# Performance work log

Hardware: AMD Instinct MI355X
Metric: run time of the kernel (lower is better)

The kernel has to match this reference:

```python
import jax, jax.numpy as jnp
import numpy as np

N, D_IN, D_OUT = 16384, 1024, 1024
E, R, TOP_K = 8, 16, 2
ALPHA = 32.0
SCALING = ALPHA / R  # standard LoRA scaling alpha/rank


def setup_inputs() -> dict:
    key = jax.random.key(0)
    k_tok, k_wb, k_a, k_b, k_g = jax.random.split(key, 5)
    tokens = jax.random.normal(k_tok, (N, D_IN), dtype=jnp.float32)
    # frozen attention projection
    W_base = jax.random.normal(k_wb, (D_IN, D_OUT), dtype=jnp.float32) * (1.0 / np.sqrt(D_IN))
    # per-expert LoRA factors
    A = jax.random.normal(k_a, (E, D_IN, R), dtype=jnp.float32) * 0.02
    B = jax.random.normal(k_b, (E, R, D_OUT), dtype=jnp.float32) * 0.02
    # router
    W_gate = jax.random.normal(k_g, (D_IN, E), dtype=jnp.float32) * (1.0 / np.sqrt(D_IN))
    return {"tokens": tokens, "W_base": W_base, "A": A, "B": B, "W_gate": W_gate}


def reference(tokens, W_base, A, B, W_gate):
    # Router: top-k gating with softmax over the selected logits
    router_logits = tokens @ W_gate                      # [N, E]
    topk_vals, selected_experts = jax.lax.top_k(router_logits, TOP_K)  # [N, K]
    expert_weights = jax.nn.softmax(topk_vals, axis=-1)  # [N, K]

    # Dense combine weights: zeros except selected experts
    gates = jnp.zeros((tokens.shape[0], E), dtype=tokens.dtype)
    gates = gates.at[jnp.arange(tokens.shape[0])[:, None], selected_experts].set(expert_weights)  # [N, E]

    # Frozen base projection
    base_out = tokens @ W_base                           # [N, D_out]

    # LoRA experts: low-rank intermediate [N, E, R] is small (rank 16)
    h = jnp.einsum('nd,edr->ner', tokens, A)             # [N, E, R]
    h = h * gates[:, :, None]                            # gate before expanding to D_out
    lora_out = jnp.einsum('ner,erm->nm', h, B)           # [N, D_out]

    out = base_out + SCALING * lora_out
    return out, router_logits, selected_experts, expert_weights
```

## Files before the change

kernel.cpp:

```cpp
#include <hip/hip_runtime.h>
#include <hip/hip_bf16.h>
#include <cstdint>
#include <cfloat>

#define NTOK 16384
#define DIN  1024
#define DOUT 1024
#define NEXP 8
#define RLORA 16
#define KTOT 1152
#define SCALE_LORA 2.0f

typedef __attribute__((ext_vector_type(8))) short bf16x8;
typedef __attribute__((ext_vector_type(4))) float f32x4;

__device__ __forceinline__ unsigned short f2bf(float f) {
  __hip_bfloat16 h = __float2bfloat16(f);
  unsigned short u;
  __builtin_memcpy(&u, &h, 2);
  return u;
}

__device__ __forceinline__ void gld_lds16(const void* g, void* l) {
  __builtin_amdgcn_global_load_lds((const __attribute__((address_space(1))) void*)g,
                                   (__attribute__((address_space(3))) void*)l,
                                   16, 0, 0);
}

__global__ __launch_bounds__(256) void k_transW(const float* __restrict__ Wb,
                                                const float* __restrict__ B,
                                                unsigned short* __restrict__ WcatT) {
  __shared__ unsigned short T[64][66];
  const int k0 = blockIdx.x * 64, j0 = blockIdx.y * 64;
  const int t = threadIdx.x;
#pragma unroll
  for (int p = 0; p < 4; ++p) {
    int kk = p * 16 + (t >> 4);
    int c4 = (t & 15) * 4;
    int k = k0 + kk;
    const float* src = (k < 1024) ? (Wb + (size_t)k * 1024) : (B + (size_t)(k - 1024) * 1024);
    float4 v = *(const float4*)(src + j0 + c4);
    T[kk][c4 + 0] = f2bf(v.x); T[kk][c4 + 1] = f2bf(v.y);
    T[kk][c4 + 2] = f2bf(v.z); T[kk][c4 + 3] = f2bf(v.w);
  }
  __syncthreads();
#pragma unroll
  for (int p = 0; p < 2; ++p) {
    int jj = p * 32 + (t >> 3);
    int kc = (t & 7) * 8;
    unsigned short buf[8];
#pragma unroll
    for (int i = 0; i < 8; ++i) buf[i] = T[kc + i][jj];
    uint4 u; __builtin_memcpy(&u, buf, 16);
    *(uint4*)(WcatT + (size_t)(j0 + jj) * KTOT + k0 + kc) = u;
  }
}

__global__ __launch_bounds__(256) void k_transA(const float* __restrict__ A,
                                                unsigned short* __restrict__ AcatT) {
  __shared__ unsigned short T[256][17];
  const int e = blockIdx.y, d0 = blockIdx.x * 256;
  const int t = threadIdx.x;
#pragma unroll
  for (int p = 0; p < 4; ++p) {
    int idx = p * 256 + t;
    int d = idx >> 2;
    int rr = (idx & 3) * 4;
    float4 v = *(const float4*)(A + (size_t)e * 16384 + (size_t)(d0 + d) * 16 + rr);
    T[d][rr + 0] = f2bf(v.x); T[d][rr + 1] = f2bf(v.y);
    T[d][rr + 2] = f2bf(v.z); T[d][rr + 3] = f2bf(v.w);
  }
  __syncthreads();
#pragma unroll
  for (int p = 0; p < 2; ++p) {
    int slot = p * 256 + t;
    int r = slot >> 5;
    int dc = (slot & 31) * 8;
    unsigned short buf[8];
#pragma unroll
    for (int i = 0; i < 8; ++i) buf[i] = T[dc + i][r];
    uint4 u; __builtin_memcpy(&u, buf, 16);
    *(uint4*)(AcatT + (size_t)(e * 16 + r) * 1024 + d0 + dc) = u;
  }
}

__global__ __launch_bounds__(256) void k_transG(const float* __restrict__ Wg,
                                                float* __restrict__ WgT) {
  int d = blockIdx.x * 256 + threadIdx.x;
  float4 a = *(const float4*)(Wg + (size_t)d * 8);
  float4 b = *(const float4*)(Wg + (size_t)d * 8 + 4);
  WgT[0 * 1024 + d] = a.x; WgT[1 * 1024 + d] = a.y;
  WgT[2 * 1024 + d] = a.z; WgT[3 * 1024 + d] = a.w;
  WgT[4 * 1024 + d] = b.x; WgT[5 * 1024 + d] = b.y;
  WgT[6 * 1024 + d] = b.z; WgT[7 * 1024 + d] = b.w;
}

__global__ __launch_bounds__(256) void k_router(const float* __restrict__ tokens,
                                                const float* __restrict__ WgT,
                                                float* __restrict__ out_logits,
                                                float* __restrict__ out_sel,
                                                float* __restrict__ out_w,
                                                unsigned short* __restrict__ Xcat,
                                                float4* __restrict__ gateinfo) {
  const int wid = threadIdx.x >> 6;
  const int lane = threadIdx.x & 63;
  const int t0 = (blockIdx.x * 4 + wid) * 2;

  float4 xa[4], xb[4];
  const float* x0 = tokens + (size_t)t0 * DIN;
  const float* x1 = x0 + DIN;
#pragma unroll
  for (int j = 0; j < 4; ++j) {
    xa[j] = *(const float4*)(x0 + j * 256 + lane * 4);
    xb[j] = *(const float4*)(x1 + j * 256 + lane * 4);
  }

#pragma unroll
  for (int tt = 0; tt < 2; ++tt) {
    unsigned short* xbp = Xcat + (size_t)(t0 + tt) * KTOT;
    const float4* xv = tt ? xb : xa;
#pragma unroll
    for (int j = 0; j < 4; ++j) {
      const float* xf = (const float*)&xv[j];
      unsigned short hb[4];
#pragma unroll
      for (int m = 0; m < 4; ++m) hb[m] = f2bf(xf[m]);
      uint2 u;
      __builtin_memcpy(&u, hb, 8);
      *(uint2*)(xbp + j * 256 + lane * 4) = u;
    }
  }

  float accA[8] = {0,0,0,0,0,0,0,0}, accB[8] = {0,0,0,0,0,0,0,0};
#pragma unroll
  for (int j = 0; j < 4; ++j) {
#pragma unroll
    for (int e = 0; e < 8; ++e) {
      float4 wv = *(const float4*)(WgT + (size_t)e * 1024 + j * 256 + lane * 4);
      accA[e] = fmaf(xa[j].x, wv.x, fmaf(xa[j].y, wv.y,
                fmaf(xa[j].z, wv.z, fmaf(xa[j].w, wv.w, accA[e]))));
      accB[e] = fmaf(xb[j].x, wv.x, fmaf(xb[j].y, wv.y,
                fmaf(xb[j].z, wv.z, fmaf(xb[j].w, wv.w, accB[e]))));
    }
  }
#pragma unroll
  for (int s = 1; s < 64; s <<= 1) {
#pragma unroll
    for (int e = 0; e < 8; ++e) {
      accA[e] += __shfl_xor(accA[e], s, 64);
      accB[e] += __shfl_xor(accB[e], s, 64);
    }
  }

#pragma unroll
  for (int tt = 0; tt < 2; ++tt) {
    const float* acc = tt ? accB : accA;
    int t = t0 + tt;
    float v0 = -FLT_MAX, v1 = -FLT_MAX;
    int i0 = -1, i1 = -1;
#pragma unroll
    for (int e = 0; e < 8; ++e) {
      float v = acc[e];
      if (v > v0) { v1 = v0; i1 = i0; v0 = v; i0 = e; }
      else if (v > v1) { v1 = v; i1 = e; }
    }
    float ex = expf(v1 - v0);
    float inv = 1.0f / (1.0f + ex);
    float w0 = inv, w1 = ex * inv;
    if (lane == 0) {
      float4* lg = (float4*)(out_logits + (size_t)t * 8);
      lg[0] = make_float4(acc[0], acc[1], acc[2], acc[3]);
      lg[1] = make_float4(acc[4], acc[5], acc[6], acc[7]);
      *(float2*)(out_sel + (size_t)t * 2) = make_float2((float)i0, (float)i1);
      *(float2*)(out_w + (size_t)t * 2) = make_float2(w0, w1);
      gateinfo[t] = make_float4((float)i0, (float)i1, w0 * SCALE_LORA, w1 * SCALE_LORA);
    }
  }
}

__global__ __launch_bounds__(256) void k_hgemm(const unsigned short* __restrict__ Xg,
                                               const unsigned short* __restrict__ Ag,
                                               const float4* __restrict__ gateinfo,
                                               unsigned short* __restrict__ Xout) {
  constexpr int BK = 64;
  __shared__ alignas(16) unsigned short As[64 * BK];
  __shared__ alignas(16) unsigned short Bs[64 * BK];
  const int tid = threadIdx.x;
  const int lane = tid & 63;
  const int wid = tid >> 6;
  const int id = blockIdx.x;
  const int xcd = id & 7, s5 = id >> 3;
  const int n0 = (s5 & 1) * 64;
  const int m0 = (xcd * 32 + (s5 >> 1)) * 64;
  const int wm = (wid >> 1) * 32, wn = (wid & 1) * 32;
  const int quad = lane >> 4, r16 = lane & 15;

  f32x4 acc[2][2] = {};

  for (int k0 = 0; k0 < 1024; k0 += BK) {
#pragma unroll
    for (int i = 0; i < 2; ++i) {
      int s = i * 256 + tid;
      int r = s >> 3, c = s & 7;
      int q = c ^ ((r >> 1) & 7);
      gld_lds16(Xg + (size_t)(m0 + r) * KTOT + k0 + q * 8, (char*)As + s * 16);
    }
#pragma unroll
    for (int i = 0; i < 2; ++i) {
      int s = i * 256 + tid;
      int r = s >> 3, c = s & 7;
      int q = c ^ ((r >> 1) & 7);
      gld_lds16(Ag + (size_t)(n0 + r) * 1024 + k0 + q * 8, (char*)Bs + s * 16);
    }
    __syncthreads();

#pragma unroll
    for (int h = 0; h < 2; ++h) {
      bf16x8 af[2], bfr[2];
#pragma unroll
      for (int mi = 0; mi < 2; ++mi) {
        int m = wm + mi * 16 + r16;
        int slot = m * 8 + ((h * 4 + quad) ^ ((m >> 1) & 7));
        af[mi] = *(const bf16x8*)((const char*)As + slot * 16);
      }
#pragma unroll
      for (int ni = 0; ni < 2; ++ni) {
        int n = wn + ni * 16 + r16;
        int slot = n * 8 + ((h * 4 + quad) ^ ((n >> 1) & 7));
        bfr[ni] = *(const bf16x8*)((const char*)Bs + slot * 16);
      }
#pragma unroll
      for (int mi = 0; mi < 2; ++mi)
#pragma unroll
        for (int ni = 0; ni < 2; ++ni)
          acc[mi][ni] = __builtin_amdgcn_mfma_f32_16x16x32_bf16(af[mi], bfr[ni], acc[mi][ni], 0, 0, 0);
    }
    __syncthreads();
  }

#pragma unroll
  for (int mi = 0; mi < 2; ++mi)
#pragma unroll
    for (int r = 0; r < 4; ++r) {
      int row = m0 + wm + mi * 16 + quad * 4 + r;
      float4 gi = gateinfo[row];
      int ie0 = (int)gi.x, ie1 = (int)gi.y;
#pragma unroll
      for (int ni = 0; ni < 2; ++ni) {
        int c = n0 + wn + ni * 16 + r16;
        int e = c >> 4;
        float h = acc[mi][ni][r];
        float v = (e == ie0) ? gi.z * h : ((e == ie1) ? gi.w * h : 0.f);
        Xout[(size_t)row * KTOT + 1024 + c] = f2bf(v);
      }
    }
}

__global__ __launch_bounds__(512, 2) void k_gemm_main(const unsigned short* __restrict__ Xg,
                                                      const unsigned short* __restrict__ Wg,
                                                      float* __restrict__ C) {
  __shared__ alignas(16) unsigned short As[2][256 * 64];
  __shared__ alignas(16) unsigned short Bs[2][256 * 64];
  const int tid = threadIdx.x;
  const int lane = tid & 63;
  const int wid = tid >> 6;
  const int id = blockIdx.x;
  const int xcd = id & 7, loc = id >> 3;
  const int gid = xcd * 32 + loc;
  const int m0 = (gid >> 2) * 256;
  const int n0 = (gid & 3) * 256;
  const int wm = (wid >> 2) * 128, wn = (wid & 3) * 64;
  const int quad = lane >> 4, r16 = lane & 15;

  f32x4 acc[8][4] = {};
  constexpr int NK = KTOT / 64;

#define STAGE(d, kt)                                                          \
  {                                                                           \
    const int k0s = (kt) * 64;                                                \
    _Pragma("unroll")                                                         \
    for (int i = 0; i < 4; ++i) {                                             \
      int s = i * 512 + tid;                                                  \
      int r = s >> 3, c = s & 7;                                              \
      int q = c ^ ((r >> 1) & 7);                                             \
      gld_lds16(Xg + (size_t)(m0 + r) * KTOT + k0s + q * 8,                   \
                (char*)As[d] + s * 16);                                       \
    }                                                                         \
    _Pragma("unroll")                                                         \
    for (int i = 0; i < 4; ++i) {                                             \
      int s = i * 512 + tid;                                                  \
      int r = s >> 3, c = s & 7;                                              \
      int q = c ^ ((r >> 1) & 7);                                             \
      gld_lds16(Wg + (size_t)(n0 + r) * KTOT + k0s + q * 8,                   \
                (char*)Bs[d] + s * 16);                                       \
    }                                                                         \
  }

  STAGE(0, 0);
  int cur = 0;
  for (int t = 0; t < NK; ++t) {
    int kt = t + 1 < NK ? t + 1 : NK - 1;
    STAGE(cur ^ 1, kt);
    asm volatile("s_waitcnt vmcnt(8)" ::: "memory");
    __builtin_amdgcn_s_barrier();

    const char* Ab = (const char*)As[cur];
    const char* Bb = (const char*)Bs[cur];
#pragma unroll
    for (int h = 0; h < 2; ++h) {
      bf16x8 af[8], bfr[4];
#pragma unroll
      for (int mi = 0; mi < 8; ++mi) {
        int m = wm + mi * 16 + r16;
        int slot = m * 8 + ((h * 4 + quad) ^ ((m >> 1) & 7));
        af[mi] = *(const bf16x8*)(Ab + slot * 16);
      }
#pragma unroll
      for (int ni = 0; ni < 4; ++ni) {
        int n = wn + ni * 16 + r16;
        int slot = n * 8 + ((h * 4 + quad) ^ ((n >> 1) & 7));
        bfr[ni] = *(const bf16x8*)(Bb + slot * 16);
      }
      __builtin_amdgcn_s_setprio(1);
#pragma unroll
      for (int mi = 0; mi < 8; ++mi)
#pragma unroll
        for (int ni = 0; ni < 4; ++ni)
          acc[mi][ni] = __builtin_amdgcn_mfma_f32_16x16x32_bf16(af[mi], bfr[ni], acc[mi][ni], 0, 0, 0);
      __builtin_amdgcn_s_setprio(0);
    }
    asm volatile("" ::: "memory");
    __builtin_amdgcn_s_barrier();
    cur ^= 1;
  }
  asm volatile("s_waitcnt vmcnt(0)" ::: "memory");
#undef STAGE

#pragma unroll
  for (int mi = 0; mi < 8; ++mi)
#pragma unroll
    for (int ni = 0; ni < 4; ++ni)
#pragma unroll
      for (int r = 0; r < 4; ++r) {
        int row = m0 + wm + mi * 16 + quad * 4 + r;
        int cc = n0 + wn + ni * 16 + r16;
        C[(size_t)row * 1024 + cc] = acc[mi][ni][r];
      }
}

extern "C" void kernel_launch(void* const* d_in, const int* in_sizes, int n_in,
                              void* d_out, int out_size, void* d_ws, size_t ws_size,
                              hipStream_t stream) {
  const float* tokens = (const float*)d_in[0];
  const float* Wb     = (const float*)d_in[1];
  const float* A      = (const float*)d_in[2];
  const float* B      = (const float*)d_in[3];
  const float* Wg     = (const float*)d_in[4];
  float* out = (float*)d_out;

  char* ws = (char*)d_ws;
  unsigned short* Xcat  = (unsigned short*)(ws);
  unsigned short* WcatT = (unsigned short*)(ws + 37748736);
  unsigned short* AcatT = (unsigned short*)(ws + 40108032);
  float4*         ginfo = (float4*)(ws + 40370176);
  float*          WgT   = (float*)(ws + 40632320);

  float* out_logits = out + (size_t)16384 * 1024;
  float* out_sel    = out_logits + (size_t)16384 * 8;
  float* out_w      = out_sel + (size_t)16384 * 2;

  k_transW<<<dim3(18, 16), dim3(256), 0, stream>>>(Wb, B, WcatT);
  k_transA<<<dim3(4, 8), dim3(256), 0, stream>>>(A, AcatT);
  k_transG<<<dim3(4), dim3(256), 0, stream>>>(Wg, WgT);
  k_router<<<dim3(2048), dim3(256), 0, stream>>>(tokens, WgT, out_logits, out_sel, out_w, Xcat, ginfo);
  k_hgemm<<<dim3(512), dim3(256), 0, stream>>>(Xcat, AcatT, ginfo, Xcat);
  k_gemm_main<<<dim3(256), dim3(512), 0, stream>>>(Xcat, WcatT, out);
}
```

Baseline: 187.9 us.

## Split GEMM tile into quadrant phases with interleaved half-tile prefetch; merge prep kernels

The main bf16 GEMM now splits each 256x256 tile into four 128x128 quadrants, each with its own LDS half-buffers. It runs an eight-phase schedule per two k-steps, issuing global-to-LDS loads for individual halves between MFMA phases with finer barriers and waitcnts, instead of one full double-buffered stage per k-step. The goal is to overlap memory traffic with MFMA work more evenly and lower register pressure per phase. The three small weight-transpose kernels are also merged into one launch to cut launch overhead. The tradeoff is more barriers per k-step and a fragile hand-tuned vmcnt ordering.

```diff
diff --git a/kernel.cpp b/kernel.cpp
--- a/kernel.cpp
+++ b/kernel.cpp
@@ -27,72 +27,73 @@
                                    16, 0, 0);
 }
 
-__global__ __launch_bounds__(256) void k_transW(const float* __restrict__ Wb,
-                                                const float* __restrict__ B,
-                                                unsigned short* __restrict__ WcatT) {
-  __shared__ unsigned short T[64][66];
-  const int k0 = blockIdx.x * 64, j0 = blockIdx.y * 64;
+__global__ __launch_bounds__(256) void k_prep(const float* __restrict__ Wb,
+                                              const float* __restrict__ B,
+                                              const float* __restrict__ A,
+                                              const float* __restrict__ Wg,
+                                              unsigned short* __restrict__ WcatT,
+                                              unsigned short* __restrict__ AcatT,
+                                              float* __restrict__ WgT) {
+  __shared__ unsigned short Tbuf[256 * 17];
+  const int bid = blockIdx.x;
   const int t = threadIdx.x;
-#pragma unroll
-  for (int p = 0; p < 4; ++p) {
-    int kk = p * 16 + (t >> 4);
-    int c4 = (t & 15) * 4;
-    int k = k0 + kk;
-    const float* src = (k < 1024) ? (Wb + (size_t)k * 1024) : (B + (size_t)(k - 1024) * 1024);
-    float4 v = *(const float4*)(src + j0 + c4);
-    T[kk][c4 + 0] = f2bf(v.x); T[kk][c4 + 1] = f2bf(v.y);
-    T[kk][c4 + 2] = f2bf(v.z); T[kk][c4 + 3] = f2bf(v.w);
-  }
-  __syncthreads();
-#pragma unroll
-  for (int p = 0; p < 2; ++p) {
-    int jj = p * 32 + (t >> 3);
-    int kc = (t & 7) * 8;
-    unsigned short buf[8];
-#pragma unroll
-    for (int i = 0; i < 8; ++i) buf[i] = T[kc + i][jj];
-    uint4 u; __builtin_memcpy(&u, buf, 16);
-    *(uint4*)(WcatT + (size_t)(j0 + jj) * KTOT + k0 + kc) = u;
-  }
-}
-
-__global__ __launch_bounds__(256) void k_transA(const float* __restrict__ A,
-                                                unsigned short* __restrict__ AcatT) {
-  __shared__ unsigned short T[256][17];
-  const int e = blockIdx.y, d0 = blockIdx.x * 256;
-  const int t = threadIdx.x;
-#pragma unroll
-  for (int p = 0; p < 4; ++p) {
-    int idx = p * 256 + t;
-    int d = idx >> 2;
-    int rr = (idx & 3) * 4;
-    float4 v = *(const float4*)(A + (size_t)e * 16384 + (size_t)(d0 + d) * 16 + rr);
-    T[d][rr + 0] = f2bf(v.x); T[d][rr + 1] = f2bf(v.y);
-    T[d][rr + 2] = f2bf(v.z); T[d][rr + 3] = f2bf(v.w);
-  }
-  __syncthreads();
-#pragma unroll
-  for (int p = 0; p < 2; ++p) {
-    int slot = p * 256 + t;
-    int r = slot >> 5;
-    int dc = (slot & 31) * 8;
-    unsigned short buf[8];
-#pragma unroll
-    for (int i = 0; i < 8; ++i) buf[i] = T[dc + i][r];
-    uint4 u; __builtin_memcpy(&u, buf, 16);
-    *(uint4*)(AcatT + (size_t)(e * 16 + r) * 1024 + d0 + dc) = u;
-  }
-}
-
-__global__ __launch_bounds__(256) void k_transG(const float* __restrict__ Wg,
-                                                float* __restrict__ WgT) {
-  int d = blockIdx.x * 256 + threadIdx.x;
-  float4 a = *(const float4*)(Wg + (size_t)d * 8);
-  float4 b = *(const float4*)(Wg + (size_t)d * 8 + 4);
-  WgT[0 * 1024 + d] = a.x; WgT[1 * 1024 + d] = a.y;
-  WgT[2 * 1024 + d] = a.z; WgT[3 * 1024 + d] = a.w;
-  WgT[4 * 1024 + d] = b.x; WgT[5 * 1024 + d] = b.y;
-  WgT[6 * 1024 + d] = b.z; WgT[7 * 1024 + d] = b.w;
+  if (bid < 288) {
+    unsigned short (*T)[66] = (unsigned short (*)[66])Tbuf;
+    const int k0 = (bid % 18) * 64, j0 = (bid / 18) * 64;
+#pragma unroll
+    for (int p = 0; p < 4; ++p) {
+      int kk = p * 16 + (t >> 4);
+      int c4 = (t & 15) * 4;
+      int k = k0 + kk;
+      const float* src = (k < 1024) ? (Wb + (size_t)k * 1024) : (B + (size_t)(k - 1024) * 1024);
+      float4 v = *(const float4*)(src + j0 + c4);
+      T[kk][c4 + 0] = f2bf(v.x); T[kk][c4 + 1] = f2bf(v.y);
+      T[kk][c4 + 2] = f2bf(v.z); T[kk][c4 + 3] = f2bf(v.w);
+    }
+    __syncthreads();
+#pragma unroll
+    for (int p = 0; p < 2; ++p) {
+      int jj = p * 32 + (t >> 3);
+      int kc = (t & 7) * 8;
+      unsigned short buf[8];
+#pragma unroll
+      for (int i = 0; i < 8; ++i) buf[i] = T[kc + i][jj];
+      uint4 u; __builtin_memcpy(&u, buf, 16);
+      *(uint4*)(WcatT + (size_t)(j0 + jj) * KTOT + k0 + kc) = u;
+    }
+  } else if (bid < 320) {
+    unsigned short (*T)[17] = (unsigned short (*)[17])Tbuf;
+    const int e = (bid - 288) >> 2, d0 = ((bid - 288) & 3) * 256;
+#pragma unroll
+    for (int p = 0; p < 4; ++p) {
+      int idx = p * 256 + t;
+      int d = idx >> 2;
+      int rr = (idx & 3) * 4;
+      float4 v = *(const float4*)(A + (size_t)e * 16384 + (size_t)(d0 + d) * 16 + rr);
+      T[d][rr + 0] = f2bf(v.x); T[d][rr + 1] = f2bf(v.y);
+      T[d][rr + 2] = f2bf(v.z); T[d][rr + 3] = f2bf(v.w);
+    }
+    __syncthreads();
+#pragma unroll
+    for (int p = 0; p < 2; ++p) {
+      int slot = p * 256 + t;
+      int r = slot >> 5;
+      int dc = (slot & 31) * 8;
+      unsigned short buf[8];
+#pragma unroll
+      for (int i = 0; i < 8; ++i) buf[i] = T[dc + i][r];
+      uint4 u; __builtin_memcpy(&u, buf, 16);
+      *(uint4*)(AcatT + (size_t)(e * 16 + r) * 1024 + d0 + dc) = u;
+    }
+  } else {
+    int d = (bid - 320) * 256 + t;
+    float4 a = *(const float4*)(Wg + (size_t)d * 8);
+    float4 b = *(const float4*)(Wg + (size_t)d * 8 + 4);
+    WgT[0 * 1024 + d] = a.x; WgT[1 * 1024 + d] = a.y;
+    WgT[2 * 1024 + d] = a.z; WgT[3 * 1024 + d] = a.w;
+    WgT[4 * 1024 + d] = b.x; WgT[5 * 1024 + d] = b.y;
+    WgT[6 * 1024 + d] = b.z; WgT[7 * 1024 + d] = b.w;
+  }
 }
 
 __global__ __launch_bounds__(256) void k_router(const float* __restrict__ tokens,
@@ -257,10 +258,10 @@
 }
 
 __global__ __launch_bounds__(512, 2) void k_gemm_main(const unsigned short* __restrict__ Xg,
-                                                      const unsigned short* __restrict__ Wg,
+                                                      const unsigned short* __restrict__ Wgm,
                                                       float* __restrict__ C) {
-  __shared__ alignas(16) unsigned short As[2][256 * 64];
-  __shared__ alignas(16) unsigned short Bs[2][256 * 64];
+  __shared__ alignas(16) unsigned short As[2][2][128 * 64];
+  __shared__ alignas(16) unsigned short Bs[2][2][128 * 64];
   const int tid = threadIdx.x;
   const int lane = tid & 63;
   const int wid = tid >> 6;
@@ -269,83 +270,113 @@
   const int gid = xcd * 32 + loc;
   const int m0 = (gid >> 2) * 256;
   const int n0 = (gid & 3) * 256;
-  const int wm = (wid >> 2) * 128, wn = (wid & 3) * 64;
+  const int wr64 = (wid >> 2) * 64;
+  const int wc32 = (wid & 3) * 32;
   const int quad = lane >> 4, r16 = lane & 15;
 
-  f32x4 acc[8][4] = {};
-  constexpr int NK = KTOT / 64;
-
-#define STAGE(d, kt)                                                          \
+  f32x4 acc[2][2][4][2] = {};
+
+#define STAGE_A(SL, HF, KT)                                                   \
   {                                                                           \
-    const int k0s = (kt) * 64;                                                \
     _Pragma("unroll")                                                         \
-    for (int i = 0; i < 4; ++i) {                                             \
-      int s = i * 512 + tid;                                                  \
-      int r = s >> 3, c = s & 7;                                              \
-      int q = c ^ ((r >> 1) & 7);                                             \
-      gld_lds16(Xg + (size_t)(m0 + r) * KTOT + k0s + q * 8,                   \
-                (char*)As[d] + s * 16);                                       \
+    for (int i_ = 0; i_ < 2; ++i_) {                                          \
+      int s_ = i_ * 512 + tid;                                                \
+      int r_ = s_ >> 3, c_ = s_ & 7;                                          \
+      int q_ = c_ ^ ((r_ >> 1) & 7);                                          \
+      gld_lds16(Xg + (size_t)(m0 + (HF) * 128 + r_) * KTOT + (KT) * 64 + q_ * 8, \
+                (char*)As[SL][HF] + s_ * 16);                                 \
+    }                                                                         \
+  }
+#define STAGE_B(SL, HF, KT)                                                   \
+  {                                                                           \
+    _Pragma("unroll")                                                         \
+    for (int i_ = 0; i_ < 2; ++i_) {                                          \
+      int s_ = i_ * 512 + tid;                                                \
+      int r_ = s_ >> 3, c_ = s_ & 7;                                          \
+      int q_ = c_ ^ ((r_ >> 1) & 7);                                          \
+      gld_lds16(Wgm + (size_t)(n0 + (HF) * 128 + r_) * KTOT + (KT) * 64 + q_ * 8, \
+                (char*)Bs[SL][HF] + s_ * 16);                                 \
+    }                                                                         \
+  }
+
+#define PHASE(SL, MH, NH, ...)                                                \
+  {                                                                           \
+    bf16x8 af[4][2], bfr[2][2];                                               \
+    const char* Ab = (const char*)As[SL][MH];                                 \
+    const char* Bb = (const char*)Bs[SL][NH];                                 \
+    _Pragma("unroll")                                                         \
+    for (int mi = 0; mi < 4; ++mi) {                                          \
+      int rh = wr64 + mi * 16 + r16;                                          \
+      int sw = (rh >> 1) & 7;                                                 \
+      af[mi][0] = *(const bf16x8*)(Ab + (rh * 8 + (quad ^ sw)) * 16);         \
+      af[mi][1] = *(const bf16x8*)(Ab + (rh * 8 + ((4 + quad) ^ sw)) * 16);   \
     }                                                                         \
     _Pragma("unroll")                                                         \
-    for (int i = 0; i < 4; ++i) {                                             \
-      int s = i * 512 + tid;                                                  \
-      int r = s >> 3, c = s & 7;                                              \
-      int q = c ^ ((r >> 1) & 7);                                             \
-      gld_lds16(Wg + (size_t)(n0 + r) * KTOT + k0s + q * 8,                   \
-                (char*)Bs[d] + s * 16);                                       \
+    for (int ni = 0; ni < 2; ++ni) {                                          \
+      int rh = wc32 + ni * 16 + r16;                                          \
+      int sw = (rh >> 1) & 7;                                                 \
+      bfr[ni][0] = *(const bf16x8*)(Bb + (rh * 8 + (quad ^ sw)) * 16);        \
+      bfr[ni][1] = *(const bf16x8*)(Bb + (rh * 8 + ((4 + quad) ^ sw)) * 16);  \
     }                                                                         \
-  }
-
-  STAGE(0, 0);
-  int cur = 0;
-  for (int t = 0; t < NK; ++t) {
-    int kt = t + 1 < NK ? t + 1 : NK - 1;
-    STAGE(cur ^ 1, kt);
-    asm volatile("s_waitcnt vmcnt(8)" ::: "memory");
-    __builtin_amdgcn_s_barrier();
-
-    const char* Ab = (const char*)As[cur];
-    const char* Bb = (const char*)Bs[cur];
-#pragma unroll
-    for (int h = 0; h < 2; ++h) {
-      bf16x8 af[8], bfr[4];
-#pragma unroll
-      for (int mi = 0; mi < 8; ++mi) {
-        int m = wm + mi * 16 + r16;
-        int slot = m * 8 + ((h * 4 + quad) ^ ((m >> 1) & 7));
-        af[mi] = *(const bf16x8*)(Ab + slot * 16);
-      }
-#pragma unroll
-      for (int ni = 0; ni < 4; ++ni) {
-        int n = wn + ni * 16 + r16;
-        int slot = n * 8 + ((h * 4 + quad) ^ ((n >> 1) & 7));
-        bfr[ni] = *(const bf16x8*)(Bb + slot * 16);
-      }
-      __builtin_amdgcn_s_setprio(1);
-#pragma unroll
-      for (int mi = 0; mi < 8; ++mi)
-#pragma unroll
-        for (int ni = 0; ni < 4; ++ni)
-          acc[mi][ni] = __builtin_amdgcn_mfma_f32_16x16x32_bf16(af[mi], bfr[ni], acc[mi][ni], 0, 0, 0);
-      __builtin_amdgcn_s_setprio(0);
-    }
-    asm volatile("" ::: "memory");
-    __builtin_amdgcn_s_barrier();
-    cur ^= 1;
+    __VA_ARGS__;                                                              \
+    asm volatile("" ::: "memory");                                            \
+    __builtin_amdgcn_s_barrier();                                             \
+    asm volatile("s_waitcnt lgkmcnt(0)" ::: "memory");                        \
+    __builtin_amdgcn_sched_barrier(0);                                        \
+    __builtin_amdgcn_s_setprio(1);                                            \
+    _Pragma("unroll")                                                         \
+    for (int mi = 0; mi < 4; ++mi)                                            \
+      _Pragma("unroll")                                                       \
+      for (int ni = 0; ni < 2; ++ni) {                                        \
+        acc[MH][NH][mi][ni] = __builtin_amdgcn_mfma_f32_16x16x32_bf16(        \
+            af[mi][0], bfr[ni][0], acc[MH][NH][mi][ni], 0, 0, 0);             \
+        acc[MH][NH][mi][ni] = __builtin_amdgcn_mfma_f32_16x16x32_bf16(        \
+            af[mi][1], bfr[ni][1], acc[MH][NH][mi][ni], 0, 0, 0);             \
+      }                                                                       \
+    __builtin_amdgcn_s_setprio(0);                                            \
+    asm volatile("" ::: "memory");                                            \
+    __builtin_amdgcn_s_barrier();                                             \
+  }
+
+  STAGE_A(0, 0, 0); STAGE_A(0, 1, 0); STAGE_B(0, 0, 0); STAGE_B(0, 1, 0);
+  STAGE_A(1, 1, 1);
+  asm volatile("s_waitcnt vmcnt(2)" ::: "memory");
+  __builtin_amdgcn_s_barrier();
+
+  for (int it = 0; it < 9; ++it) {
+    const int kt1 = 2 * it + 1;
+    const int kt2 = (2 * it + 2 < 18) ? 2 * it + 2 : 17;
+    const int kt3 = (2 * it + 3 < 18) ? 2 * it + 3 : 17;
+    PHASE(0, 0, 0, STAGE_A(1, 0, kt1); STAGE_B(1, 0, kt1))
+    PHASE(0, 1, 1, STAGE_B(1, 1, kt1))
+    PHASE(0, 1, 0, )
+    PHASE(0, 0, 1, STAGE_A(0, 1, kt2);
+                   asm volatile("s_waitcnt vmcnt(2)" ::: "memory"))
+    PHASE(1, 0, 0, STAGE_A(0, 0, kt2); STAGE_B(0, 0, kt2))
+    PHASE(1, 1, 1, STAGE_B(0, 1, kt2))
+    PHASE(1, 1, 0, )
+    PHASE(1, 0, 1, STAGE_A(1, 1, kt3);
+                   asm volatile("s_waitcnt vmcnt(2)" ::: "memory"))
   }
   asm volatile("s_waitcnt vmcnt(0)" ::: "memory");
-#undef STAGE
-
-#pragma unroll
-  for (int mi = 0; mi < 8; ++mi)
-#pragma unroll
-    for (int ni = 0; ni < 4; ++ni)
-#pragma unroll
-      for (int r = 0; r < 4; ++r) {
-        int row = m0 + wm + mi * 16 + quad * 4 + r;
-        int cc = n0 + wn + ni * 16 + r16;
-        C[(size_t)row * 1024 + cc] = acc[mi][ni][r];
-      }
+#undef PHASE
+#undef STAGE_A
+#undef STAGE_B
+
+#pragma unroll
+  for (int mh = 0; mh < 2; ++mh)
+#pragma unroll
+    for (int nh = 0; nh < 2; ++nh)
+#pragma unroll
+      for (int mi = 0; mi < 4; ++mi)
+#pragma unroll
+        for (int ni = 0; ni < 2; ++ni)
+#pragma unroll
+          for (int r = 0; r < 4; ++r) {
+            int row = m0 + mh * 128 + wr64 + mi * 16 + quad * 4 + r;
+            int cc = n0 + nh * 128 + wc32 + ni * 16 + r16;
+            C[(size_t)row * 1024 + cc] = acc[mh][nh][mi][ni][r];
+          }
 }
 
 extern "C" void kernel_launch(void* const* d_in, const int* in_sizes, int n_in,
@@ -369,9 +400,7 @@
   float* out_sel    = out_logits + (size_t)16384 * 8;
   float* out_w      = out_sel + (size_t)16384 * 2;
 
-  k_transW<<<dim3(18, 16), dim3(256), 0, stream>>>(Wb, B, WcatT);
-  k_transA<<<dim3(4, 8), dim3(256), 0, stream>>>(A, AcatT);
-  k_transG<<<dim3(4), dim3(256), 0, stream>>>(Wg, WgT);
+  k_prep<<<dim3(324), dim3(256), 0, stream>>>(Wb, B, A, Wg, WcatT, AcatT, WgT);
   k_router<<<dim3(2048), dim3(256), 0, stream>>>(tokens, WgT, out_logits, out_sel, out_w, Xcat, ginfo);
   k_hgemm<<<dim3(512), dim3(256), 0, stream>>>(Xcat, AcatT, ginfo, Xcat);
   k_gemm_main<<<dim3(256), dim3(512), 0, stream>>>(Xcat, WcatT, out);
```

After: 186.1 us. About the same (-0.9%).

## Merge weight-prep kernels and switch main GEMM to 128x128 single-buffered tiles

Applied to the files above, without the earlier changes.

The three weight transpose/convert kernels become one launch whose blocks pick their task by block index, removing two kernel launches. The main bf16 GEMM changes from 256x256 tiles with 512 threads and double-buffered LDS prefetch to 128x128 tiles with 256 threads, a single LDS buffer and plain __syncthreads. This targets higher occupancy (4 blocks per CU) and more blocks across the device. In exchange it gives up overlap of global loads with MFMA work, and the smaller tiles reuse each loaded operand less.

```diff
diff --git a/kernel.cpp b/kernel.cpp
--- a/kernel.cpp
+++ b/kernel.cpp
@@ -27,72 +27,73 @@
                                    16, 0, 0);
 }
 
-__global__ __launch_bounds__(256) void k_transW(const float* __restrict__ Wb,
-                                                const float* __restrict__ B,
-                                                unsigned short* __restrict__ WcatT) {
-  __shared__ unsigned short T[64][66];
-  const int k0 = blockIdx.x * 64, j0 = blockIdx.y * 64;
+__global__ __launch_bounds__(256) void k_prep(const float* __restrict__ Wb,
+                                              const float* __restrict__ B,
+                                              const float* __restrict__ A,
+                                              const float* __restrict__ Wg,
+                                              unsigned short* __restrict__ WcatT,
+                                              unsigned short* __restrict__ AcatT,
+                                              float* __restrict__ WgT) {
+  __shared__ unsigned short Tbuf[256 * 17];
+  const int bid = blockIdx.x;
   const int t = threadIdx.x;
-#pragma unroll
-  for (int p = 0; p < 4; ++p) {
-    int kk = p * 16 + (t >> 4);
-    int c4 = (t & 15) * 4;
-    int k = k0 + kk;
-    const float* src = (k < 1024) ? (Wb + (size_t)k * 1024) : (B + (size_t)(k - 1024) * 1024);
-    float4 v = *(const float4*)(src + j0 + c4);
-    T[kk][c4 + 0] = f2bf(v.x); T[kk][c4 + 1] = f2bf(v.y);
-    T[kk][c4 + 2] = f2bf(v.z); T[kk][c4 + 3] = f2bf(v.w);
-  }
-  __syncthreads();
-#pragma unroll
-  for (int p = 0; p < 2; ++p) {
-    int jj = p * 32 + (t >> 3);
-    int kc = (t & 7) * 8;
-    unsigned short buf[8];
-#pragma unroll
-    for (int i = 0; i < 8; ++i) buf[i] = T[kc + i][jj];
-    uint4 u; __builtin_memcpy(&u, buf, 16);
-    *(uint4*)(WcatT + (size_t)(j0 + jj) * KTOT + k0 + kc) = u;
-  }
-}
-
-__global__ __launch_bounds__(256) void k_transA(const float* __restrict__ A,
-                                                unsigned short* __restrict__ AcatT) {
-  __shared__ unsigned short T[256][17];
-  const int e = blockIdx.y, d0 = blockIdx.x * 256;
-  const int t = threadIdx.x;
-#pragma unroll
-  for (int p = 0; p < 4; ++p) {
-    int idx = p * 256 + t;
-    int d = idx >> 2;
-    int rr = (idx & 3) * 4;
-    float4 v = *(const float4*)(A + (size_t)e * 16384 + (size_t)(d0 + d) * 16 + rr);
-    T[d][rr + 0] = f2bf(v.x); T[d][rr + 1] = f2bf(v.y);
-    T[d][rr + 2] = f2bf(v.z); T[d][rr + 3] = f2bf(v.w);
-  }
-  __syncthreads();
-#pragma unroll
-  for (int p = 0; p < 2; ++p) {
-    int slot = p * 256 + t;
-    int r = slot >> 5;
-    int dc = (slot & 31) * 8;
-    unsigned short buf[8];
-#pragma unroll
-    for (int i = 0; i < 8; ++i) buf[i] = T[dc + i][r];
-    uint4 u; __builtin_memcpy(&u, buf, 16);
-    *(uint4*)(AcatT + (size_t)(e * 16 + r) * 1024 + d0 + dc) = u;
-  }
-}
-
-__global__ __launch_bounds__(256) void k_transG(const float* __restrict__ Wg,
-                                                float* __restrict__ WgT) {
-  int d = blockIdx.x * 256 + threadIdx.x;
-  float4 a = *(const float4*)(Wg + (size_t)d * 8);
-  float4 b = *(const float4*)(Wg + (size_t)d * 8 + 4);
-  WgT[0 * 1024 + d] = a.x; WgT[1 * 1024 + d] = a.y;
-  WgT[2 * 1024 + d] = a.z; WgT[3 * 1024 + d] = a.w;
-  WgT[4 * 1024 + d] = b.x; WgT[5 * 1024 + d] = b.y;
-  WgT[6 * 1024 + d] = b.z; WgT[7 * 1024 + d] = b.w;
+  if (bid < 288) {
+    unsigned short (*T)[66] = (unsigned short (*)[66])Tbuf;
+    const int k0 = (bid % 18) * 64, j0 = (bid / 18) * 64;
+#pragma unroll
+    for (int p = 0; p < 4; ++p) {
+      int kk = p * 16 + (t >> 4);
+      int c4 = (t & 15) * 4;
+      int k = k0 + kk;
+      const float* src = (k < 1024) ? (Wb + (size_t)k * 1024) : (B + (size_t)(k - 1024) * 1024);
+      float4 v = *(const float4*)(src + j0 + c4);
+      T[kk][c4 + 0] = f2bf(v.x); T[kk][c4 + 1] = f2bf(v.y);
+      T[kk][c4 + 2] = f2bf(v.z); T[kk][c4 + 3] = f2bf(v.w);
+    }
+    __syncthreads();
+#pragma unroll
+    for (int p = 0; p < 2; ++p) {
+      int jj = p * 32 + (t >> 3);
+      int kc = (t & 7) * 8;
+      unsigned short buf[8];
+#pragma unroll
+      for (int i = 0; i < 8; ++i) buf[i] = T[kc + i][jj];
+      uint4 u; __builtin_memcpy(&u, buf, 16);
+      *(uint4*)(WcatT + (size_t)(j0 + jj) * KTOT + k0 + kc) = u;
+    }
+  } else if (bid < 320) {
+    unsigned short (*T)[17] = (unsigned short (*)[17])Tbuf;
+    const int e = (bid - 288) >> 2, d0 = ((bid - 288) & 3) * 256;
+#pragma unroll
+    for (int p = 0; p < 4; ++p) {
+      int idx = p * 256 + t;
+      int d = idx >> 2;
+      int rr = (idx & 3) * 4;
+      float4 v = *(const float4*)(A + (size_t)e * 16384 + (size_t)(d0 + d) * 16 + rr);
+      T[d][rr + 0] = f2bf(v.x); T[d][rr + 1] = f2bf(v.y);
+      T[d][rr + 2] = f2bf(v.z); T[d][rr + 3] = f2bf(v.w);
+    }
+    __syncthreads();
+#pragma unroll
+    for (int p = 0; p < 2; ++p) {
+      int slot = p * 256 + t;
+      int r = slot >> 5;
+      int dc = (slot & 31) * 8;
+      unsigned short buf[8];
+#pragma unroll
+      for (int i = 0; i < 8; ++i) buf[i] = T[dc + i][r];
+      uint4 u; __builtin_memcpy(&u, buf, 16);
+      *(uint4*)(AcatT + (size_t)(e * 16 + r) * 1024 + d0 + dc) = u;
+    }
+  } else {
+    int d = (bid - 320) * 256 + t;
+    float4 a = *(const float4*)(Wg + (size_t)d * 8);
+    float4 b = *(const float4*)(Wg + (size_t)d * 8 + 4);
+    WgT[0 * 1024 + d] = a.x; WgT[1 * 1024 + d] = a.y;
+    WgT[2 * 1024 + d] = a.z; WgT[3 * 1024 + d] = a.w;
+    WgT[4 * 1024 + d] = b.x; WgT[5 * 1024 + d] = b.y;
+    WgT[6 * 1024 + d] = b.z; WgT[7 * 1024 + d] = b.w;
+  }
 }
 
 __global__ __launch_bounds__(256) void k_router(const float* __restrict__ tokens,
@@ -256,88 +257,67 @@
     }
 }
 
-__global__ __launch_bounds__(512, 2) void k_gemm_main(const unsigned short* __restrict__ Xg,
-                                                      const unsigned short* __restrict__ Wg,
+__global__ __launch_bounds__(256, 4) void k_gemm_main(const unsigned short* __restrict__ Xg,
+                                                      const unsigned short* __restrict__ Wgm,
                                                       float* __restrict__ C) {
-  __shared__ alignas(16) unsigned short As[2][256 * 64];
-  __shared__ alignas(16) unsigned short Bs[2][256 * 64];
+  __shared__ alignas(16) unsigned short As[128 * 64];
+  __shared__ alignas(16) unsigned short Bs[128 * 64];
   const int tid = threadIdx.x;
   const int lane = tid & 63;
   const int wid = tid >> 6;
   const int id = blockIdx.x;
-  const int xcd = id & 7, loc = id >> 3;
-  const int gid = xcd * 32 + loc;
-  const int m0 = (gid >> 2) * 256;
-  const int n0 = (gid & 3) * 256;
-  const int wm = (wid >> 2) * 128, wn = (wid & 3) * 64;
+  const int gid = (id & 7) * 128 + (id >> 3);
+  const int m0 = (gid >> 3) * 128;
+  const int n0 = (gid & 7) * 128;
+  const int wm = (wid >> 1) * 64, wn = (wid & 1) * 64;
   const int quad = lane >> 4, r16 = lane & 15;
 
-  f32x4 acc[8][4] = {};
-  constexpr int NK = KTOT / 64;
-
-#define STAGE(d, kt)                                                          \
-  {                                                                           \
-    const int k0s = (kt) * 64;                                                \
-    _Pragma("unroll")                                                         \
-    for (int i = 0; i < 4; ++i) {                                             \
-      int s = i * 512 + tid;                                                  \
-      int r = s >> 3, c = s & 7;                                              \
-      int q = c ^ ((r >> 1) & 7);                                             \
-      gld_lds16(Xg + (size_t)(m0 + r) * KTOT + k0s + q * 8,                   \
-                (char*)As[d] + s * 16);                                       \
-    }                                                                         \
-    _Pragma("unroll")                                                         \
-    for (int i = 0; i < 4; ++i) {                                             \
-      int s = i * 512 + tid;                                                  \
-      int r = s >> 3, c = s & 7;                                              \
-      int q = c ^ ((r >> 1) & 7);                                             \
-      gld_lds16(Wg + (size_t)(n0 + r) * KTOT + k0s + q * 8,                   \
-                (char*)Bs[d] + s * 16);                                       \
-    }                                                                         \
-  }
-
-  STAGE(0, 0);
-  int cur = 0;
-  for (int t = 0; t < NK; ++t) {
-    int kt = t + 1 < NK ? t + 1 : NK - 1;
-    STAGE(cur ^ 1, kt);
-    asm volatile("s_waitcnt vmcnt(8)" ::: "memory");
-    __builtin_amdgcn_s_barrier();
-
-    const char* Ab = (const char*)As[cur];
-    const char* Bb = (const char*)Bs[cur];
+  f32x4 acc[4][4] = {};
+
+  for (int kt = 0; kt < 18; ++kt) {
+    const int k0 = kt * 64;
+#pragma unroll
+    for (int i = 0; i < 4; ++i) {
+      int s = i * 256 + tid;
+      int r = s >> 3, c = s & 7;
+      int q = c ^ ((r >> 1) & 7);
+      gld_lds16(Xg + (size_t)(m0 + r) * KTOT + k0 + q * 8, (char*)As + s * 16);
+    }
+#pragma unroll
+    for (int i = 0; i < 4; ++i) {
+      int s = i * 256 + tid;
+      int r = s >> 3, c = s & 7;
+      int q = c ^ ((r >> 1) & 7);
+      gld_lds16(Wgm + (size_t)(n0 + r) * KTOT + k0 + q * 8, (char*)Bs + s * 16);
+    }
+    __syncthreads();
+
 #pragma unroll
     for (int h = 0; h < 2; ++h) {
-      bf16x8 af[8], bfr[4];
-#pragma unroll
-      for (int mi = 0; mi < 8; ++mi) {
+      bf16x8 af[4], bfr[4];
+#pragma unroll
+      for (int mi = 0; mi < 4; ++mi) {
         int m = wm + mi * 16 + r16;
         int slot = m * 8 + ((h * 4 + quad) ^ ((m >> 1) & 7));
-        af[mi] = *(const bf16x8*)(Ab + slot * 16);
+        af[mi] = *(const bf16x8*)((const char*)As + slot * 16);
       }
 #pragma unroll
       for (int ni = 0; ni < 4; ++ni) {
         int n = wn + ni * 16 + r16;
         int slot = n * 8 + ((h * 4 + quad) ^ ((n >> 1) & 7));
-        bfr[ni] = *(const bf16x8*)(Bb + slot * 16);
-      }
-      __builtin_amdgcn_s_setprio(1);
-#pragma unroll
-      for (int mi = 0; mi < 8; ++mi)
+        bfr[ni] = *(const bf16x8*)((const char*)Bs + slot * 16);
+      }
+#pragma unroll
+      for (int mi = 0; mi < 4; ++mi)
 #pragma unroll
         for (int ni = 0; ni < 4; ++ni)
           acc[mi][ni] = __builtin_amdgcn_mfma_f32_16x16x32_bf16(af[mi], bfr[ni], acc[mi][ni], 0, 0, 0);
-      __builtin_amdgcn_s_setprio(0);
-    }
-    asm volatile("" ::: "memory");
-    __builtin_amdgcn_s_barrier();
-    cur ^= 1;
-  }
-  asm volatile("s_waitcnt vmcnt(0)" ::: "memory");
-#undef STAGE
-
-#pragma unroll
-  for (int mi = 0; mi < 8; ++mi)
+    }
+    __syncthreads();
+  }
+
+#pragma unroll
+  for (int mi = 0; mi < 4; ++mi)
 #pragma unroll
     for (int ni = 0; ni < 4; ++ni)
 #pragma unroll
@@ -369,10 +349,8 @@
   float* out_sel    = out_logits + (size_t)16384 * 8;
   float* out_w      = out_sel + (size_t)16384 * 2;
 
-  k_transW<<<dim3(18, 16), dim3(256), 0, stream>>>(Wb, B, WcatT);
-  k_transA<<<dim3(4, 8), dim3(256), 0, stream>>>(A, AcatT);
-  k_transG<<<dim3(4), dim3(256), 0, stream>>>(Wg, WgT);
+  k_prep<<<dim3(324), dim3(256), 0, stream>>>(Wb, B, A, Wg, WcatT, AcatT, WgT);
   k_router<<<dim3(2048), dim3(256), 0, stream>>>(tokens, WgT, out_logits, out_sel, out_w, Xcat, ginfo);
   k_hgemm<<<dim3(512), dim3(256), 0, stream>>>(Xcat, AcatT, ginfo, Xcat);
-  k_gemm_main<<<dim3(256), dim3(512), 0, stream>>>(Xcat, WcatT, out);
-}
+  k_gemm_main<<<dim3(1024), dim3(256), 0, stream>>>(Xcat, WcatT, out);
+}
```

Measured after the change: 180.4 us. 4.0% less time.
